# Kernel tuning notes

Hardware: AMD Instinct MI355X
Metric: run time of the kernel (lower is better)

## Reference

```python
import jax, jax.numpy as jnp
import numpy as np

D = 128        # d_model
B = 32         # graphs in batch
NV = 500       # vars per graph -> 2*NV literals per graph
NL = B * 2 * NV            # 32000 literals
NC_G = 2000                # clauses per graph
NC = B * NC_G              # 64000 clauses
K = 3                      # literals per clause
NE = NC * K                # 192000 edges


def setup_inputs() -> dict:
    key = jax.random.key(0)
    ks = jax.random.split(key, 16)
    s = 1.0 / np.sqrt(D)
    inp = {
        'x_unk': jax.random.uniform(ks[0], (NL, D), dtype=jnp.float32),
        'C_w': jax.random.normal(ks[1], (D,), dtype=jnp.float32) * s,
        'C_b': jax.random.normal(ks[2], (D,), dtype=jnp.float32) * s,
        'Wih_lc': jax.random.normal(ks[3], (4 * D, D), dtype=jnp.float32) * s,
        'Whh_lc': jax.random.normal(ks[4], (4 * D, D), dtype=jnp.float32) * s,
        'bih_lc': jax.random.normal(ks[5], (4 * D,), dtype=jnp.float32) * s,
        'bhh_lc': jax.random.normal(ks[6], (4 * D,), dtype=jnp.float32) * s,
        'Wih_cl': jax.random.normal(ks[7], (4 * D, 2 * D), dtype=jnp.float32) * s,
        'Whh_cl': jax.random.normal(ks[8], (4 * D, D), dtype=jnp.float32) * s,
        'bih_cl': jax.random.normal(ks[9], (4 * D,), dtype=jnp.float32) * s,
        'bhh_cl': jax.random.normal(ks[10], (4 * D,), dtype=jnp.float32) * s,
        'out_w': jax.random.normal(ks[11], (D, 1), dtype=jnp.float32) * s,
        'out_b': jax.random.normal(ks[12], (1,), dtype=jnp.float32) * s,
    }
    rng = np.random.default_rng(0)
    # each clause samples K literals within its own graph
    lit_local = rng.integers(0, 2 * NV, size=(B, NC_G, K))
    offs = (np.arange(B) * 2 * NV)[:, None, None]
    inp['lit_idx'] = jnp.asarray((lit_local + offs).reshape(-1), dtype=jnp.int32)
    inp['clause_idx'] = jnp.asarray(np.repeat(np.arange(NC), K), dtype=jnp.int32)
    inp['l_batch'] = jnp.asarray(np.repeat(np.arange(B), 2 * NV), dtype=jnp.int32)
    # literal flip: swap pos/neg halves within each graph
    loc = np.arange(2 * NV)
    flip_local = np.concatenate([loc[NV:], loc[:NV]])
    inp['flip_perm'] = jnp.asarray(((np.arange(B) * 2 * NV)[:, None] + flip_local[None, :]).reshape(-1), dtype=jnp.int32)
    inp['num_iters'] = 4
    return inp


def _lstm_step(x, h, c, Wih, Whh, bih, bhh):
    # PyTorch LSTM cell: gates ordered [i, f, g, o]
    g = x @ Wih.T + h @ Whh.T + (bih + bhh)
    i, f, gg, o = jnp.split(g, 4, axis=-1)
    c2 = jax.nn.sigmoid(f) * c + jax.nn.sigmoid(i) * jnp.tanh(gg)
    h2 = jax.nn.sigmoid(o) * jnp.tanh(c2)
    return h2, c2


def reference(x_unk, C_w, C_b, Wih_lc, Whh_lc, bih_lc, bhh_lc,
              Wih_cl, Whh_cl, bih_cl, bhh_cl, out_w, out_b,
              clause_idx, lit_idx, l_batch, flip_perm, num_iters):
    n_lits = x_unk.shape[0]
    n_clauses = clause_idx.shape[0] // K
    # init embeddings: x_unk ~ U[0,1); x_c = C_init(1) repeated; cell states zero
    h_l, c_l = x_unk, jnp.zeros_like(x_unk)
    h_c = jnp.broadcast_to(C_w + C_b, (n_clauses, D))  # Linear(1,d) on ones(1)
    c_c = jnp.zeros((n_clauses, D), dtype=x_unk.dtype)
    for _ in range(num_iters):
        # lit -> clause: msg = adj_t @ x_l (SpMM via gather+segment_sum)
        msg_c = jax.ops.segment_sum(h_l[lit_idx], clause_idx, num_segments=n_clauses)
        h_c, c_c = _lstm_step(msg_c, h_c, c_c, Wih_lc, Whh_lc, bih_lc, bhh_lc)
        # clause -> lit: msg = adj_t.T @ x_c, concat with flipped literals
        msg_l = jax.ops.segment_sum(h_c[clause_idx], lit_idx, num_segments=n_lits)
        inp = jnp.concatenate([msg_l, h_l[flip_perm]], axis=-1)  # [NL, 2D]
        h_l, c_l = _lstm_step(inp, h_l, c_l, Wih_cl, Whh_cl, bih_cl, bhh_cl)
    votes = h_l @ out_w + out_b  # [NL, 1]
    sums = jax.ops.segment_sum(votes, l_batch, num_segments=B)
    cnts = jax.ops.segment_sum(jnp.ones((n_lits, 1), votes.dtype), l_batch, num_segments=B)
    vote_reduced = sums / cnts  # global_mean_pool
    return vote_reduced, votes, h_l
```

## Files before the change

kernel.cpp:

```cpp
#include <hip/hip_runtime.h>
#include <hip/hip_bf16.h>

#define D     128
#define NLIT  32000
#define NCLA  64000
#define KLIT  3
#define NEDGE 192000
#define BGR   32
#define ITERS 4
#define LITS_PER_GRAPH 1000

typedef _Float16 f16x8 __attribute__((ext_vector_type(8)));
typedef float    f32x4 __attribute__((ext_vector_type(4)));

#define TSTRIDE 40

__device__ __forceinline__ float sigf(float x)  { return 1.f / (1.f + __expf(-x)); }
__device__ __forceinline__ float tanhft(float x){ return 1.f - 2.f / (__expf(2.f * x) + 1.f); }

__global__ void conv_x_kernel(const float* __restrict__ x, _Float16* __restrict__ o) {
    int t = blockIdx.x * blockDim.x + threadIdx.x;
    if (t >= NLIT * 16) return;
    const float* p = x + t * 8;
    f16x8 v;
#pragma unroll
    for (int i = 0; i < 8; ++i) v[i] = (_Float16)p[i];
    *(f16x8*)((_Float16*)o + t * 8) = v;
}

__global__ void conv_wc_kernel(const float* __restrict__ Wih,
                               const float* __restrict__ Whh,
                               _Float16* __restrict__ Wc) {
    int n = blockIdx.x, k = threadIdx.x;
    float v = (k < 128) ? Wih[n * 128 + k] : Whh[n * 128 + k - 128];
    Wc[n * 256 + k] = (_Float16)v;
}

__global__ void conv_wl_kernel(const float* __restrict__ Wih,
                               const float* __restrict__ Whh,
                               _Float16* __restrict__ Wl) {
    int n = blockIdx.x, k = threadIdx.x;
    float v = (k < 256) ? Wih[n * 256 + k] : Whh[n * 128 + k - 256];
    Wl[n * 384 + k] = (_Float16)v;
}

__global__ void conv_bias_kernel(const float* bih_c, const float* bhh_c, float* bc,
                                 const float* bih_l, const float* bhh_l, float* bl,
                                 const float* C_w, const float* C_b,
                                 _Float16* hc0g) {
    int t = threadIdx.x;
    bc[t] = bih_c[t] + bhh_c[t];
    bl[t] = bih_l[t] + bhh_l[t];
    if (t < 128) hc0g[t] = (_Float16)(C_w[t] + C_b[t]);
}

__global__ void count_edges_kernel(const int* __restrict__ lit_idx,
                                   int* __restrict__ counts) {
    int e = blockIdx.x * blockDim.x + threadIdx.x;
    if (e < NEDGE) atomicAdd(&counts[lit_idx[e]], 1);
}

__global__ __launch_bounds__(256)
void block_sum_kernel(const int* __restrict__ counts, int* __restrict__ bsum) {
    int b = blockIdx.x, t = threadIdx.x;
    int v = counts[b * 256 + t];
    int lane = t & 63, w = t >> 6;
#pragma unroll
    for (int off = 32; off > 0; off >>= 1) v += __shfl_down(v, off, 64);
    __shared__ int ws[4];
    if (lane == 0) ws[w] = v;
    __syncthreads();
    if (t == 0) bsum[b] = ws[0] + ws[1] + ws[2] + ws[3];
}

__global__ void scan_bsum_kernel(const int* __restrict__ bsum,
                                 int* __restrict__ ebsum,
                                 int* __restrict__ starts) {
    __shared__ int s[128];
    int t = threadIdx.x;
    int v = (t < 125) ? bsum[t] : 0;
    s[t] = v;
    __syncthreads();
    for (int off = 1; off < 128; off <<= 1) {
        int y = (t >= off) ? s[t - off] : 0;
        __syncthreads();
        s[t] += y;
        __syncthreads();
    }
    if (t < 125) ebsum[t] = s[t] - v;
    if (t == 0) starts[NLIT] = NEDGE;
}

__global__ __launch_bounds__(256)
void scan_write_kernel(const int* __restrict__ counts,
                       const int* __restrict__ ebsum,
                       int* __restrict__ starts,
                       int* __restrict__ cursor) {
    int b = blockIdx.x, t = threadIdx.x;
    int idx = b * 256 + t;
    int v = counts[idx];
    int lane = t & 63, w = t >> 6;
    int x = v;
#pragma unroll
    for (int off = 1; off < 64; off <<= 1) {
        int y = __shfl_up(x, off, 64);
        if (lane >= off) x += y;
    }
    __shared__ int wsum[4];
    if (lane == 63) wsum[w] = x;
    __syncthreads();
    int woff = 0;
#pragma unroll
    for (int i = 0; i < 4; ++i) if (i < w) woff += wsum[i];
    int g = ebsum[b] + woff + x - v;
    starts[idx] = g;
    cursor[idx] = g;
}

__global__ void fill_csr_kernel(const int* __restrict__ lit_idx,
                                const int* __restrict__ clause_idx,
                                int* __restrict__ cursor,
                                int* __restrict__ edge_clause) {
    int e = blockIdx.x * blockDim.x + threadIdx.x;
    if (e < NEDGE) {
        int l = lit_idx[e];
        int pos = atomicAdd(&cursor[l], 1);
        edge_clause[pos] = clause_idx[e];
    }
}

__global__ void gather_msg_kernel(const _Float16* __restrict__ h_c16,
                                  _Float16* __restrict__ msg16,
                                  const int* __restrict__ starts,
                                  const int* __restrict__ edge_clause) {
    int t = blockIdx.x * blockDim.x + threadIdx.x;
    if (t >= NLIT * 16) return;
    int l = t >> 4;
    int off = (t & 15) * 8;
    int s = starts[l], e = starts[l + 1];
    float a[8];
#pragma unroll
    for (int i = 0; i < 8; ++i) a[i] = 0.f;
    for (int j = s; j < e; ++j) {
        f16x8 v = *(const f16x8*)&h_c16[(size_t)edge_clause[j] * D + off];
#pragma unroll
        for (int i = 0; i < 8; ++i) a[i] += (float)v[i];
    }
    f16x8 o;
#pragma unroll
    for (int i = 0; i < 8; ++i) o[i] = (_Float16)a[i];
    *(f16x8*)&msg16[(size_t)l * D + off] = o;
}

__global__ __launch_bounds__(256, 2)
void clause_mfma_kernel(const _Float16* __restrict__ h_l16,
                        const _Float16* __restrict__ h_c_old,
                        _Float16* __restrict__ h_c_new,
                        _Float16* __restrict__ c_c16,
                        const _Float16* __restrict__ Wc,
                        const float* __restrict__ bc,
                        const _Float16* __restrict__ hc0g,
                        const int* __restrict__ lit_idx,
                        int first) {
    __shared__ _Float16 Wt[256 * TSTRIDE];
    __shared__ _Float16 At[128 * TSTRIDE];
    __shared__ int      lidx[384];

    const int tid  = threadIdx.x;
    const int w    = tid >> 6;
    const int lane = tid & 63;
    const int qd   = lane >> 4;
    const int ln   = lane & 15;
    const int c    = blockIdx.x & 1;
    const int row0 = (blockIdx.x >> 1) * 128;

    for (int i = tid; i < 384; i += 256) lidx[i] = lit_idx[row0 * 3 + i];
    __syncthreads();

    f16x8 ldW[4];
    f16x8 ldG[2][3];

#pragma unroll
    for (int jj = 0; jj < 4; ++jj) {
        int gg = tid + 256 * jj;
        int tr = gg >> 2, col8 = (gg & 3) * 8;
        int grow = (tr >> 6) * 128 + c * 64 + (tr & 63);
        ldW[jj] = *(const f16x8*)&Wc[grow * 256 + col8];
    }
#pragma unroll
    for (int s2 = 0; s2 < 2; ++s2) {
        int s = tid + 256 * s2;
        int m = s >> 2, col8 = (s & 3) * 8;
#pragma unroll
        for (int r = 0; r < 3; ++r)
            ldG[s2][r] = *(const f16x8*)&h_l16[(size_t)lidx[3 * m + r] * D + col8];
    }

    f32x4 acc[8][4];
#pragma unroll
    for (int R = 0; R < 8; ++R)
#pragma unroll
        for (int g = 0; g < 4; ++g) { acc[R][g][0]=0.f; acc[R][g][1]=0.f; acc[R][g][2]=0.f; acc[R][g][3]=0.f; }

    for (int ch = 0; ch < 8; ++ch) {
        if (ch) __syncthreads();
#pragma unroll
        for (int jj = 0; jj < 4; ++jj) {
            int gg = tid + 256 * jj;
            int tr = gg >> 2, col8 = (gg & 3) * 8;
            *(f16x8*)&Wt[tr * TSTRIDE + col8] = ldW[jj];
        }
#pragma unroll
        for (int s2 = 0; s2 < 2; ++s2) {
            int s = tid + 256 * s2;
            int m = s >> 2, col8 = (s & 3) * 8;
            if (ch < 4) {
                f16x8 o;
#pragma unroll
                for (int e = 0; e < 8; ++e)
                    o[e] = (_Float16)((float)ldG[s2][0][e] + (float)ldG[s2][1][e] + (float)ldG[s2][2][e]);
                *(f16x8*)&At[m * TSTRIDE + col8] = o;
            } else {
                *(f16x8*)&At[m * TSTRIDE + col8] = ldG[s2][0];
            }
        }
        if (ch < 7) {
            const int k0n = (ch + 1) * 32;
#pragma unroll
            for (int jj = 0; jj < 4; ++jj) {
                int gg = tid + 256 * jj;
                int tr = gg >> 2, col8 = (gg & 3) * 8;
                int grow = (tr >> 6) * 128 + c * 64 + (tr & 63);
                ldW[jj] = *(const f16x8*)&Wc[grow * 256 + k0n + col8];
            }
            if (ch + 1 < 4) {
#pragma unroll
                for (int s2 = 0; s2 < 2; ++s2) {
                    int s = tid + 256 * s2;
                    int m = s >> 2, col8 = (s & 3) * 8;
#pragma unroll
                    for (int r = 0; r < 3; ++r)
                        ldG[s2][r] = *(const f16x8*)&h_l16[(size_t)lidx[3 * m + r] * D + k0n + col8];
                }
            } else {
                const int kk = k0n - 128;
#pragma unroll
                for (int s2 = 0; s2 < 2; ++s2) {
                    int s = tid + 256 * s2;
                    int m = s >> 2, col8 = (s & 3) * 8;
                    ldG[s2][0] = first ? *(const f16x8*)&hc0g[kk + col8]
                                       : *(const f16x8*)&h_c_old[(size_t)(row0 + m) * D + kk + col8];
                }
            }
        }
        __syncthreads();
        f16x8 af[8], bf[4];
#pragma unroll
        for (int R = 0; R < 8; ++R)
            af[R] = *(const f16x8*)&At[(16 * R + ln) * TSTRIDE + qd * 8];
#pragma unroll
        for (int g = 0; g < 4; ++g)
            bf[g] = *(const f16x8*)&Wt[(64 * g + 16 * w + ln) * TSTRIDE + qd * 8];
#pragma unroll
        for (int R = 0; R < 8; ++R)
#pragma unroll
            for (int g = 0; g < 4; ++g)
                acc[R][g] = __builtin_amdgcn_mfma_f32_16x16x32_f16(af[R], bf[g], acc[R][g], 0, 0, 0);
    }

    const int dcol = c * 64 + 16 * w + ln;
    const float b0 = bc[dcol], b1 = bc[128 + dcol], b2 = bc[256 + dcol], b3 = bc[384 + dcol];
#pragma unroll
    for (int R = 0; R < 8; ++R) {
#pragma unroll
        for (int r = 0; r < 4; ++r) {
            int m = row0 + 16 * R + qd * 4 + r;
            size_t idx = (size_t)m * D + dcol;
            float gi = acc[R][0][r] + b0;
            float gf = acc[R][1][r] + b1;
            float gg = acc[R][2][r] + b2;
            float go = acc[R][3][r] + b3;
            float cn = sigf(gi) * tanhft(gg);
            if (!first) cn += sigf(gf) * (float)c_c16[idx];
            float h  = sigf(go) * tanhft(cn);
            c_c16[idx]   = (_Float16)cn;
            h_c_new[idx] = (_Float16)h;
        }
    }
}

__global__ __launch_bounds__(256, 2)
void literal_mfma_kernel(const _Float16* __restrict__ h_old16,
                         const _Float16* __restrict__ msg16,
                         _Float16* __restrict__ h_new16,
                         float* __restrict__ h32,
                         _Float16* __restrict__ c_l16,
                         const _Float16* __restrict__ Wl384,
                         const float* __restrict__ bl,
                         const int* __restrict__ flip_perm,
                         int first) {
    __shared__ _Float16 Wt[256 * TSTRIDE];
    __shared__ _Float16 At[128 * TSTRIDE];
    __shared__ int      flip_s[128];

    const int tid  = threadIdx.x;
    const int w    = tid >> 6;
    const int lane = tid & 63;
    const int qd   = lane >> 4;
    const int ln   = lane & 15;
    const int c    = blockIdx.x & 1;
    const int row0 = (blockIdx.x >> 1) * 128;

    if (tid < 128) flip_s[tid] = flip_perm[row0 + tid];
    __syncthreads();

    f16x8 ldW[4];
    f16x8 ldA[2];

#pragma unroll
    for (int jj = 0; jj < 4; ++jj) {
        int gg = tid + 256 * jj;
        int tr = gg >> 2, col8 = (gg & 3) * 8;
        int grow = (tr >> 6) * 128 + c * 64 + (tr & 63);
        ldW[jj] = *(const f16x8*)&Wl384[grow * 384 + col8];
    }
#pragma unroll
    for (int s2 = 0; s2 < 2; ++s2) {
        int s = tid + 256 * s2;
        int m = s >> 2, col8 = (s & 3) * 8;
        ldA[s2] = *(const f16x8*)&msg16[(size_t)(row0 + m) * D + col8];
    }

    f32x4 acc[8][4];
#pragma unroll
    for (int R = 0; R < 8; ++R)
#pragma unroll
        for (int g = 0; g < 4; ++g) { acc[R][g][0]=0.f; acc[R][g][1]=0.f; acc[R][g][2]=0.f; acc[R][g][3]=0.f; }

    for (int ch = 0; ch < 12; ++ch) {
        if (ch) __syncthreads();
#pragma unroll
        for (int jj = 0; jj < 4; ++jj) {
            int gg = tid + 256 * jj;
            int tr = gg >> 2, col8 = (gg & 3) * 8;
            *(f16x8*)&Wt[tr * TSTRIDE + col8] = ldW[jj];
        }
#pragma unroll
        for (int s2 = 0; s2 < 2; ++s2) {
            int s = tid + 256 * s2;
            int m = s >> 2, col8 = (s & 3) * 8;
            *(f16x8*)&At[m * TSTRIDE + col8] = ldA[s2];
        }
        if (ch < 11) {
            const int k0n = (ch + 1) * 32;
#pragma unroll
            for (int jj = 0; jj < 4; ++jj) {
                int gg = tid + 256 * jj;
                int tr = gg >> 2, col8 = (gg & 3) * 8;
                int grow = (tr >> 6) * 128 + c * 64 + (tr & 63);
                ldW[jj] = *(const f16x8*)&Wl384[grow * 384 + k0n + col8];
            }
#pragma unroll
            for (int s2 = 0; s2 < 2; ++s2) {
                int s = tid + 256 * s2;
                int m = s >> 2, col8 = (s & 3) * 8;
                const _Float16* g;
                if (k0n < 128)      g = msg16   + (size_t)(row0 + m) * D + k0n + col8;
                else if (k0n < 256) g = h_old16 + (size_t)flip_s[m] * D + (k0n - 128) + col8;
                else                g = h_old16 + (size_t)(row0 + m) * D + (k0n - 256) + col8;
                ldA[s2] = *(const f16x8*)g;
            }
        }
        __syncthreads();
        f16x8 af[8], bf[4];
#pragma unroll
        for (int R = 0; R < 8; ++R)
            af[R] = *(const f16x8*)&At[(16 * R + ln) * TSTRIDE + qd * 8];
#pragma unroll
        for (int g = 0; g < 4; ++g)
            bf[g] = *(const f16x8*)&Wt[(64 * g + 16 * w + ln) * TSTRIDE + qd * 8];
#pragma unroll
        for (int R = 0; R < 8; ++R)
#pragma unroll
            for (int g = 0; g < 4; ++g)
                acc[R][g] = __builtin_amdgcn_mfma_f32_16x16x32_f16(af[R], bf[g], acc[R][g], 0, 0, 0);
    }

    const int dcol = c * 64 + 16 * w + ln;
    const float b0 = bl[dcol], b1 = bl[128 + dcol], b2 = bl[256 + dcol], b3 = bl[384 + dcol];
#pragma unroll
    for (int R = 0; R < 8; ++R) {
#pragma unroll
        for (int r = 0; r < 4; ++r) {
            int m = row0 + 16 * R + qd * 4 + r;
            size_t idx = (size_t)m * D + dcol;
            float gi = acc[R][0][r] + b0;
            float gf = acc[R][1][r] + b1;
            float gg = acc[R][2][r] + b2;
            float go = acc[R][3][r] + b3;
            float cn = sigf(gi) * tanhft(gg);
            if (!first) cn += sigf(gf) * (float)c_l16[idx];
            float h  = sigf(go) * tanhft(cn);
            c_l16[idx]   = (_Float16)cn;
            h_new16[idx] = (_Float16)h;
            if (h32) h32[idx] = h;
        }
    }
}

__global__ __launch_bounds__(256)
void votes_stage1_kernel(const float* __restrict__ h_l,
                         const float* __restrict__ out_w,
                         const float* __restrict__ out_b,
                         float* __restrict__ votes_out) {
    int w    = threadIdx.x >> 6;
    int lane = threadIdx.x & 63;
    int l    = blockIdx.x * 4 + w;
    if (l >= NLIT) return;
    const float2 v = *(const float2*)&h_l[(size_t)l * D + lane * 2];
    const float2 ww = *(const float2*)&out_w[lane * 2];
    float p = v.x * ww.x + v.y * ww.y;
#pragma unroll
    for (int off = 32; off > 0; off >>= 1) p += __shfl_down(p, off, 64);
    if (lane == 0) votes_out[l] = p + out_b[0];
}

__global__ __launch_bounds__(256)
void votes_stage2_kernel(const float* __restrict__ votes,
                         float* __restrict__ out0) {
    int b = blockIdx.x;
    int t = threadIdx.x;
    const float* base = votes + (size_t)b * LITS_PER_GRAPH;
    float s = 0.f;
    for (int i = t; i < LITS_PER_GRAPH; i += 256) s += base[i];
#pragma unroll
    for (int off = 32; off > 0; off >>= 1) s += __shfl_down(s, off, 64);
    __shared__ float ws[4];
    if ((t & 63) == 0) ws[t >> 6] = s;
    __syncthreads();
    if (t == 0) out0[b] = (ws[0] + ws[1] + ws[2] + ws[3]) / (float)LITS_PER_GRAPH;
}

extern "C" void kernel_launch(void* const* d_in, const int* in_sizes, int n_in,
                              void* d_out, int out_size, void* d_ws, size_t ws_size,
                              hipStream_t stream) {
    (void)in_sizes; (void)n_in; (void)out_size; (void)ws_size;

    const float* x_unk  = (const float*)d_in[0];
    const float* C_w    = (const float*)d_in[1];
    const float* C_b    = (const float*)d_in[2];
    const float* Wih_lc = (const float*)d_in[3];
    const float* Whh_lc = (const float*)d_in[4];
    const float* bih_lc = (const float*)d_in[5];
    const float* bhh_lc = (const float*)d_in[6];
    const float* Wih_cl = (const float*)d_in[7];
    const float* Whh_cl = (const float*)d_in[8];
    const float* bih_cl = (const float*)d_in[9];
    const float* bhh_cl = (const float*)d_in[10];
    const float* out_w  = (const float*)d_in[11];
    const float* out_b  = (const float*)d_in[12];
    const int* lit_idx    = (const int*)d_in[13];
    const int* clause_idx = (const int*)d_in[14];
    const int* flip_perm  = (const int*)d_in[16];

    char* W = (char*)d_ws;
    size_t off = 0;
    auto alloc = [&](size_t bytes) { char* p = W + off; off = (off + bytes + 255) & ~(size_t)255; return p; };
    _Float16* h_l16_0 = (_Float16*)alloc((size_t)NLIT * D * 2);
    _Float16* h_l16_1 = (_Float16*)alloc((size_t)NLIT * D * 2);
    _Float16* h_c16_0 = (_Float16*)alloc((size_t)NCLA * D * 2);
    _Float16* h_c16_1 = (_Float16*)alloc((size_t)NCLA * D * 2);
    _Float16* msg16   = (_Float16*)alloc((size_t)NLIT * D * 2);
    _Float16* c_l16   = (_Float16*)alloc((size_t)NLIT * D * 2);
    _Float16* c_c16   = (_Float16*)alloc((size_t)NCLA * D * 2);
    _Float16* Wc16    = (_Float16*)alloc(512 * 256 * 2);
    _Float16* Wl16    = (_Float16*)alloc(512 * 384 * 2);
    float*    bc      = (float*)  alloc(512 * 4);
    float*    bl      = (float*)  alloc(512 * 4);
    _Float16* hc0g    = (_Float16*)alloc(128 * 2);
    int* counts       = (int*)alloc((size_t)NLIT * 4);
    int* starts       = (int*)alloc((size_t)(NLIT + 1) * 4);
    int* cursor       = (int*)alloc((size_t)NLIT * 4);
    int* edge_clause  = (int*)alloc((size_t)NEDGE * 4);
    int* bsum         = (int*)alloc(128 * 4);
    int* ebsum        = (int*)alloc(128 * 4);

    float* out       = (float*)d_out;
    float* out_votes = out + BGR;
    float* out_hl    = out + BGR + NLIT;

    hipMemsetAsync(counts, 0, (size_t)NLIT * 4, stream);

    conv_x_kernel<<<(NLIT * 16 + 255) / 256, 256, 0, stream>>>(x_unk, h_l16_0);
    conv_wc_kernel<<<512, 256, 0, stream>>>(Wih_lc, Whh_lc, Wc16);
    conv_wl_kernel<<<512, 384, 0, stream>>>(Wih_cl, Whh_cl, Wl16);
    conv_bias_kernel<<<1, 512, 0, stream>>>(bih_lc, bhh_lc, bc, bih_cl, bhh_cl, bl,
                                            C_w, C_b, hc0g);

    count_edges_kernel<<<(NEDGE + 255) / 256, 256, 0, stream>>>(lit_idx, counts);
    block_sum_kernel<<<NLIT / 256, 256, 0, stream>>>(counts, bsum);
    scan_bsum_kernel<<<1, 128, 0, stream>>>(bsum, ebsum, starts);
    scan_write_kernel<<<NLIT / 256, 256, 0, stream>>>(counts, ebsum, starts, cursor);
    fill_csr_kernel<<<(NEDGE + 255) / 256, 256, 0, stream>>>(lit_idx, clause_idx,
                                                             cursor, edge_clause);

    const _Float16* hl_old[ITERS] = {h_l16_0, h_l16_1, h_l16_0, h_l16_1};
    _Float16*       hl_new[ITERS] = {h_l16_1, h_l16_0, h_l16_1, h_l16_0};
    const _Float16* hc_old[ITERS] = {h_c16_0, h_c16_1, h_c16_0, h_c16_1};
    _Float16*       hc_new[ITERS] = {h_c16_1, h_c16_0, h_c16_1, h_c16_0};

    for (int it = 0; it < ITERS; ++it) {
        clause_mfma_kernel<<<(NCLA / 128) * 2, 256, 0, stream>>>(
            hl_old[it], hc_old[it], hc_new[it], c_c16, Wc16, bc, hc0g, lit_idx,
            it == 0 ? 1 : 0);
        gather_msg_kernel<<<(NLIT * 16 + 255) / 256, 256, 0, stream>>>(
            hc_new[it], msg16, starts, edge_clause);
        literal_mfma_kernel<<<(NLIT / 128) * 2, 256, 0, stream>>>(
            hl_old[it], msg16, hl_new[it],
            (it == ITERS - 1) ? out_hl : (float*)nullptr,
            c_l16, Wl16, bl, flip_perm,
            it == 0 ? 1 : 0);
    }

    votes_stage1_kernel<<<NLIT / 4, 256, 0, stream>>>(out_hl, out_w, out_b, out_votes);
    votes_stage2_kernel<<<BGR, 256, 0, stream>>>(out_votes, out);
}
```

Before: 531.9 us.

## Load MFMA weight fragments directly from global into registers, drop weight LDS tile

In both the clause and literal LSTM MFMA kernels, each lane now loads its B-operand weight fragment straight from global memory (L2/L1-cached) into registers, double-buffered across k-chunks. This replaces staging the weight tile through shared memory. It removes the LDS writes and reads for weights and shrinks shared memory per block. Launch bounds are raised to 3 blocks per SM for higher occupancy. The cost is uncoalesced, per-lane strided global loads of weights, and tighter register pressure under the higher occupancy bound.

New measurement: 1.047 ms. +96.8%, slower.

```diff
diff --git a/kernel.cpp b/kernel.cpp
--- a/kernel.cpp
+++ b/kernel.cpp
@@ -152,7 +152,7 @@
     *(f16x8*)&msg16[(size_t)l * D + off] = o;
 }
 
-__global__ __launch_bounds__(256, 2)
+__global__ __launch_bounds__(256, 3)
 void clause_mfma_kernel(const _Float16* __restrict__ h_l16,
                         const _Float16* __restrict__ h_c_old,
                         _Float16* __restrict__ h_c_new,
@@ -162,7 +162,6 @@
                         const _Float16* __restrict__ hc0g,
                         const int* __restrict__ lit_idx,
                         int first) {
-    __shared__ _Float16 Wt[256 * TSTRIDE];
     __shared__ _Float16 At[128 * TSTRIDE];
     __shared__ int      lidx[384];
 
@@ -177,16 +176,15 @@
     for (int i = tid; i < 384; i += 256) lidx[i] = lit_idx[row0 * 3 + i];
     __syncthreads();
 
-    f16x8 ldW[4];
+    const int nrow = c * 64 + 16 * w + ln;
+    const int koff = qd * 8;
+
+    f16x8 ldB[4];
     f16x8 ldG[2][3];
 
 #pragma unroll
-    for (int jj = 0; jj < 4; ++jj) {
-        int gg = tid + 256 * jj;
-        int tr = gg >> 2, col8 = (gg & 3) * 8;
-        int grow = (tr >> 6) * 128 + c * 64 + (tr & 63);
-        ldW[jj] = *(const f16x8*)&Wc[grow * 256 + col8];
-    }
+    for (int g = 0; g < 4; ++g)
+        ldB[g] = *(const f16x8*)&Wc[(size_t)(g * 128 + nrow) * 256 + koff];
 #pragma unroll
     for (int s2 = 0; s2 < 2; ++s2) {
         int s = tid + 256 * s2;
@@ -204,12 +202,6 @@
 
     for (int ch = 0; ch < 8; ++ch) {
         if (ch) __syncthreads();
-#pragma unroll
-        for (int jj = 0; jj < 4; ++jj) {
-            int gg = tid + 256 * jj;
-            int tr = gg >> 2, col8 = (gg & 3) * 8;
-            *(f16x8*)&Wt[tr * TSTRIDE + col8] = ldW[jj];
-        }
 #pragma unroll
         for (int s2 = 0; s2 < 2; ++s2) {
             int s = tid + 256 * s2;
@@ -224,15 +216,14 @@
                 *(f16x8*)&At[m * TSTRIDE + col8] = ldG[s2][0];
             }
         }
+        f16x8 bf[4];
+#pragma unroll
+        for (int g = 0; g < 4; ++g) bf[g] = ldB[g];
         if (ch < 7) {
             const int k0n = (ch + 1) * 32;
 #pragma unroll
-            for (int jj = 0; jj < 4; ++jj) {
-                int gg = tid + 256 * jj;
-                int tr = gg >> 2, col8 = (gg & 3) * 8;
-                int grow = (tr >> 6) * 128 + c * 64 + (tr & 63);
-                ldW[jj] = *(const f16x8*)&Wc[grow * 256 + k0n + col8];
-            }
+            for (int g = 0; g < 4; ++g)
+                ldB[g] = *(const f16x8*)&Wc[(size_t)(g * 128 + nrow) * 256 + k0n + koff];
             if (ch + 1 < 4) {
 #pragma unroll
                 for (int s2 = 0; s2 < 2; ++s2) {
@@ -254,13 +245,10 @@
             }
         }
         __syncthreads();
-        f16x8 af[8], bf[4];
+        f16x8 af[8];
 #pragma unroll
         for (int R = 0; R < 8; ++R)
-            af[R] = *(const f16x8*)&At[(16 * R + ln) * TSTRIDE + qd * 8];
-#pragma unroll
-        for (int g = 0; g < 4; ++g)
-            bf[g] = *(const f16x8*)&Wt[(64 * g + 16 * w + ln) * TSTRIDE + qd * 8];
+            af[R] = *(const f16x8*)&At[(16 * R + ln) * TSTRIDE + koff];
 #pragma unroll
         for (int R = 0; R < 8; ++R)
 #pragma unroll
@@ -289,7 +277,7 @@
     }
 }
 
-__global__ __launch_bounds__(256, 2)
+__global__ __launch_bounds__(256, 3)
 void literal_mfma_kernel(const _Float16* __restrict__ h_old16,
                          const _Float16* __restrict__ msg16,
                          _Float16* __restrict__ h_new16,
@@ -299,7 +287,6 @@
                          const float* __restrict__ bl,
                          const int* __restrict__ flip_perm,
                          int first) {
-    __shared__ _Float16 Wt[256 * TSTRIDE];
     __shared__ _Float16 At[128 * TSTRIDE];
     __shared__ int      flip_s[128];
 
@@ -314,16 +301,15 @@
     if (tid < 128) flip_s[tid] = flip_perm[row0 + tid];
     __syncthreads();
 
-    f16x8 ldW[4];
+    const int nrow = c * 64 + 16 * w + ln;
+    const int koff = qd * 8;
+
+    f16x8 ldB[4];
     f16x8 ldA[2];
 
 #pragma unroll
-    for (int jj = 0; jj < 4; ++jj) {
-        int gg = tid + 256 * jj;
-        int tr = gg >> 2, col8 = (gg & 3) * 8;
-        int grow = (tr >> 6) * 128 + c * 64 + (tr & 63);
-        ldW[jj] = *(const f16x8*)&Wl384[grow * 384 + col8];
-    }
+    for (int g = 0; g < 4; ++g)
+        ldB[g] = *(const f16x8*)&Wl384[(size_t)(g * 128 + nrow) * 384 + koff];
 #pragma unroll
     for (int s2 = 0; s2 < 2; ++s2) {
         int s = tid + 256 * s2;
@@ -339,27 +325,20 @@
 
     for (int ch = 0; ch < 12; ++ch) {
         if (ch) __syncthreads();
-#pragma unroll
-        for (int jj = 0; jj < 4; ++jj) {
-            int gg = tid + 256 * jj;
-            int tr = gg >> 2, col8 = (gg & 3) * 8;
-            *(f16x8*)&Wt[tr * TSTRIDE + col8] = ldW[jj];
-        }
 #pragma unroll
         for (int s2 = 0; s2 < 2; ++s2) {
             int s = tid + 256 * s2;
             int m = s >> 2, col8 = (s & 3) * 8;
             *(f16x8*)&At[m * TSTRIDE + col8] = ldA[s2];
         }
+        f16x8 bf[4];
+#pragma unroll
+        for (int g = 0; g < 4; ++g) bf[g] = ldB[g];
         if (ch < 11) {
             const int k0n = (ch + 1) * 32;
 #pragma unroll
-            for (int jj = 0; jj < 4; ++jj) {
-                int gg = tid + 256 * jj;
-                int tr = gg >> 2, col8 = (gg & 3) * 8;
-                int grow = (tr >> 6) * 128 + c * 64 + (tr & 63);
-                ldW[jj] = *(const f16x8*)&Wl384[grow * 384 + k0n + col8];
-            }
+            for (int g = 0; g < 4; ++g)
+                ldB[g] = *(const f16x8*)&Wl384[(size_t)(g * 128 + nrow) * 384 + k0n + koff];
 #pragma unroll
             for (int s2 = 0; s2 < 2; ++s2) {
                 int s = tid + 256 * s2;
@@ -372,13 +351,10 @@
             }
         }
         __syncthreads();
-        f16x8 af[8], bf[4];
+        f16x8 af[8];
 #pragma unroll
         for (int R = 0; R < 8; ++R)
-            af[R] = *(const f16x8*)&At[(16 * R + ln) * TSTRIDE + qd * 8];
-#pragma unroll
-        for (int g = 0; g < 4; ++g)
-            bf[g] = *(const f16x8*)&Wt[(64 * g + 16 * w + ln) * TSTRIDE + qd * 8];
+            af[R] = *(const f16x8*)&At[(16 * R + ln) * TSTRIDE + koff];
 #pragma unroll
         for (int R = 0; R < 8; ++R)
 #pragma unroll
```
